# Performance work log

Measured on AMD Instinct MI355X. Metric: run time of the kernel, lower is better.

The kernel has to match this reference:

```python
import jax, jax.numpy as jnp
import numpy as np

N_NODES = 100000
N_EDGES = 800000
N_GRAPHS = 256
IN_C = 96
HID = 96
OUT_C = 16


def setup_inputs() -> dict:
    key = jax.random.key(0)
    ks = jax.random.split(key, 10)
    x = jax.random.normal(ks[0], (N_NODES, IN_C), dtype=jnp.float32)
    edge_index = jax.random.randint(ks[1], (2, N_EDGES), 0, N_NODES, dtype=jnp.int64)
    batch = jnp.sort(jax.random.randint(ks[2], (N_NODES,), 0, N_GRAPHS, dtype=jnp.int64))
    def glorot(k, fan_in, fan_out):
        s = np.sqrt(6.0 / (fan_in + fan_out)).astype(np.float32)
        return jax.random.uniform(k, (fan_in, fan_out), minval=-s, maxval=s, dtype=jnp.float32)
    W1 = glorot(ks[3], IN_C, HID)
    W2 = glorot(ks[4], HID, HID)
    W3 = glorot(ks[5], HID, HID)
    Wlin = glorot(ks[6], HID, OUT_C)
    b1 = jnp.zeros((HID,), dtype=jnp.float32)
    b2 = jnp.zeros((HID,), dtype=jnp.float32)
    b3 = jnp.zeros((HID,), dtype=jnp.float32)
    return {"x": x, "edge_index": edge_index, "batch": batch,
            "W1": W1, "b1": b1, "W2": W2, "b2": b2, "W3": W3, "b3": b3, "Wlin": Wlin}


def _gcn_conv(x, W, b, src, dst):
    # PyG GCNConv(normalize=True): add self-loops, deg includes self-loop,
    # norm_ij = deg_i^{-1/2} * deg_j^{-1/2}; linear (no bias) then scatter-add; bias after.
    n = x.shape[0]
    deg = jnp.zeros((n,), dtype=x.dtype).at[dst].add(1.0) + 1.0  # +1 self-loop
    dinv = jax.lax.rsqrt(deg)
    h = x @ W                                   # [N, H]
    coef = dinv[src] * dinv[dst]                # [E]
    msg = h[src] * coef[:, None]                # [E, H] gather
    agg = jax.ops.segment_sum(msg, dst, num_segments=n)  # scatter-add
    agg = agg + h * (dinv * dinv)[:, None]      # self-loop contribution
    return agg + b


def reference(x, edge_index, batch, W1, b1, W2, b2, W3, b3, Wlin):
    src, dst = edge_index[0], edge_index[1]
    h = jax.nn.relu(_gcn_conv(x, W1, b1, src, dst))
    h = jax.nn.relu(_gcn_conv(h, W2, b2, src, dst))
    h = _gcn_conv(h, W3, b3, src, dst)
    # global mean pool over graphs
    sums = jax.ops.segment_sum(h, batch, num_segments=N_GRAPHS)
    counts = jax.ops.segment_sum(jnp.ones((h.shape[0],), dtype=h.dtype), batch, num_segments=N_GRAPHS)
    pooled = sums / jnp.maximum(counts, 1.0)[:, None]
    return pooled @ Wlin
```

## Files before the change

kernel.cpp:

```cpp
#include <hip/hip_runtime.h>

#define NN 100000
#define NE 800000
#define NG 256
#define CH 96
#define OC 16
#define NBLK 391
#define TM 128
#define WPAD 104

typedef __attribute__((ext_vector_type(8))) short bf16x8;
typedef __attribute__((ext_vector_type(4))) float f32x4;

__global__ __launch_bounds__(256) void k_hist(const int* __restrict__ dst,
                                              int* __restrict__ cnt,
                                              int* __restrict__ slot) {
    int e = blockIdx.x * 256 + threadIdx.x;
    slot[e] = atomicAdd(&cnt[dst[e]], 1);
}

__global__ __launch_bounds__(256) void k_scan1(const int* __restrict__ cnt,
                                               int* __restrict__ off,
                                               int* __restrict__ bsum) {
    __shared__ int sh[256];
    int t = threadIdx.x;
    int i = blockIdx.x * 256 + t;
    int v = (i < NN) ? cnt[i] : 0;
    sh[t] = v;
    __syncthreads();
    for (int d = 1; d < 256; d <<= 1) {
        int x = (t >= d) ? sh[t - d] : 0;
        __syncthreads();
        sh[t] += x;
        __syncthreads();
    }
    if (i < NN) off[i] = sh[t] - v;
    if (t == 255) bsum[blockIdx.x] = sh[255];
}

__global__ __launch_bounds__(512) void k_scan2(int* __restrict__ bsum,
                                               int* __restrict__ boff) {
    __shared__ int sh[512];
    int t = threadIdx.x;
    int v = (t < NBLK) ? bsum[t] : 0;
    sh[t] = v;
    __syncthreads();
    for (int d = 1; d < 512; d <<= 1) {
        int x = (t >= d) ? sh[t - d] : 0;
        __syncthreads();
        sh[t] += x;
        __syncthreads();
    }
    if (t < NBLK) boff[t] = sh[t] - v;
}

__global__ __launch_bounds__(256) void k_scan3(const int* __restrict__ cnt,
                                               int* __restrict__ off,
                                               const int* __restrict__ boff,
                                               float* __restrict__ dinv,
                                               const int* __restrict__ batch,
                                               int* __restrict__ goff) {
    int i = blockIdx.x * 256 + threadIdx.x;
    if (i >= NN) return;
    off[i] += boff[i >> 8];
    dinv[i] = rsqrtf((float)cnt[i] + 1.0f);
    int b = batch[i];
    int bp = (i > 0) ? batch[i - 1] : -1;
    for (int g = bp + 1; g <= b; g++) goff[g] = i;
    if (i == NN - 1)
        for (int g = b + 1; g <= NG; g++) goff[g] = NN;
}

__global__ __launch_bounds__(256) void k_build(const int* __restrict__ src,
                                               const int* __restrict__ dst,
                                               const int* __restrict__ off,
                                               const int* __restrict__ slot,
                                               const float* __restrict__ dinv,
                                               float2* __restrict__ packed) {
    int e = blockIdx.x * 256 + threadIdx.x;
    int s = src[e];
    int d = dst[e];
    packed[off[d] + slot[e]] = make_float2(__int_as_float(s), dinv[s] * dinv[d]);
}

__device__ __forceinline__ unsigned short f2bf(float x) {
    unsigned u = __float_as_uint(x);
    return (unsigned short)((u + 0x7fffu + ((u >> 16) & 1u)) >> 16);
}
__device__ __forceinline__ float bf2f(unsigned short h) {
    return __uint_as_float(((unsigned)h) << 16);
}

__device__ __forceinline__ void split8(const float4 a, const float4 b,
                                       bf16x8& hi, bf16x8& lo) {
    float v[8] = {a.x, a.y, a.z, a.w, b.x, b.y, b.z, b.w};
#pragma unroll
    for (int j = 0; j < 8; j++) {
        unsigned short h = f2bf(v[j]);
        hi[j] = (short)h;
        lo[j] = (short)f2bf(v[j] - bf2f(h));
    }
}

__global__ __launch_bounds__(256) void k_gemm96(const float* __restrict__ X,
                                                const float* __restrict__ W,
                                                unsigned short* __restrict__ H) {
    __shared__ unsigned short WtHi[CH * WPAD];
    __shared__ unsigned short WtLo[CH * WPAD];

    const int tid = threadIdx.x;
    const int n0 = blockIdx.x * TM;

    {
        const float4* W4 = reinterpret_cast<const float4*>(W);
#pragma unroll
        for (int i = 0; i < 9; i++) {
            int f4 = tid * 9 + i;
            int k = f4 / 24;
            int nn = (f4 - k * 24) * 4;
            float4 v = W4[f4];
            float vv[4] = {v.x, v.y, v.z, v.w};
#pragma unroll
            for (int e = 0; e < 4; e++) {
                unsigned short h = f2bf(vv[e]);
                WtHi[(nn + e) * WPAD + k] = h;
                WtLo[(nn + e) * WPAD + k] = f2bf(vv[e] - bf2f(h));
            }
        }
    }
    __syncthreads();

    const int lane = tid & 63;
    const int wave = tid >> 6;
    const int lrow = lane & 15;
    const int quad = lane >> 4;

    const float4* X4 = reinterpret_cast<const float4*>(X);

    f32x4 acc[2][6];
#pragma unroll
    for (int rt = 0; rt < 2; rt++)
#pragma unroll
        for (int ct = 0; ct < 6; ct++) acc[rt][ct] = (f32x4){0.f, 0.f, 0.f, 0.f};

    int arow[2];
#pragma unroll
    for (int rt = 0; rt < 2; rt++)
        arow[rt] = min(n0 + (wave * 2 + rt) * 16 + lrow, NN - 1);

#pragma unroll
    for (int kc = 0; kc < 3; kc++) {
        bf16x8 ahi[2], alo[2];
#pragma unroll
        for (int rt = 0; rt < 2; rt++) {
            int fo = (arow[rt] * CH + kc * 32 + quad * 8) >> 2;
            split8(X4[fo], X4[fo + 1], ahi[rt], alo[rt]);
        }
#pragma unroll
        for (int ct = 0; ct < 6; ct++) {
            int bo = (ct * 16 + lrow) * WPAD + kc * 32 + quad * 8;
            bf16x8 bhi = *reinterpret_cast<const bf16x8*>(&WtHi[bo]);
            bf16x8 blo = *reinterpret_cast<const bf16x8*>(&WtLo[bo]);
#pragma unroll
            for (int rt = 0; rt < 2; rt++) {
                acc[rt][ct] = __builtin_amdgcn_mfma_f32_16x16x32_bf16(
                    alo[rt], bhi, acc[rt][ct], 0, 0, 0);
                acc[rt][ct] = __builtin_amdgcn_mfma_f32_16x16x32_bf16(
                    ahi[rt], blo, acc[rt][ct], 0, 0, 0);
                acc[rt][ct] = __builtin_amdgcn_mfma_f32_16x16x32_bf16(
                    ahi[rt], bhi, acc[rt][ct], 0, 0, 0);
            }
        }
    }

#pragma unroll
    for (int rt = 0; rt < 2; rt++) {
        int rbase = n0 + (wave * 2 + rt) * 16 + quad * 4;
#pragma unroll
        for (int ct = 0; ct < 6; ct++) {
            int col = ct * 16 + lrow;
#pragma unroll
            for (int r = 0; r < 4; r++) {
                int row = rbase + r;
                if (row < NN) H[(size_t)row * CH + col] = f2bf(acc[rt][ct][r]);
            }
        }
    }
}

__device__ __forceinline__ float4 us4_to_f4(ushort4 u) {
    return make_float4(bf2f(u.x), bf2f(u.y), bf2f(u.z), bf2f(u.w));
}

template <bool RELU>
__global__ __launch_bounds__(256) void k_aggregate(const int* __restrict__ off,
                                                   const float2* __restrict__ packed,
                                                   const float* __restrict__ dinv,
                                                   const float* __restrict__ bias,
                                                   const unsigned short* __restrict__ H,
                                                   float* __restrict__ B) {
    int idx = blockIdx.x * 256 + threadIdx.x;
    int n = idx / 24;
    int c4 = idx - n * 24;
    int e0 = off[n];
    int e1 = (n + 1 < NN) ? off[n + 1] : NE;

    const ushort4* H4 = reinterpret_cast<const ushort4*>(H);
    float di = dinv[n];
    float d2 = di * di;
    float4 h = us4_to_f4(H4[(size_t)n * 24 + c4]);
    float4 bb = reinterpret_cast<const float4*>(bias)[c4];
    float4 acc = make_float4(h.x * d2 + bb.x, h.y * d2 + bb.y,
                             h.z * d2 + bb.z, h.w * d2 + bb.w);

    int e = e0;
    for (; e + 4 <= e1; e += 4) {
        float2 p0 = packed[e + 0];
        float2 p1 = packed[e + 1];
        float2 p2 = packed[e + 2];
        float2 p3 = packed[e + 3];
        float4 v0 = us4_to_f4(H4[(size_t)__float_as_int(p0.x) * 24 + c4]);
        float4 v1 = us4_to_f4(H4[(size_t)__float_as_int(p1.x) * 24 + c4]);
        float4 v2 = us4_to_f4(H4[(size_t)__float_as_int(p2.x) * 24 + c4]);
        float4 v3 = us4_to_f4(H4[(size_t)__float_as_int(p3.x) * 24 + c4]);
        acc.x += v0.x * p0.y + v1.x * p1.y + v2.x * p2.y + v3.x * p3.y;
        acc.y += v0.y * p0.y + v1.y * p1.y + v2.y * p2.y + v3.y * p3.y;
        acc.z += v0.z * p0.y + v1.z * p1.y + v2.z * p2.y + v3.z * p3.y;
        acc.w += v0.w * p0.y + v1.w * p1.y + v2.w * p2.y + v3.w * p3.y;
    }
    for (; e < e1; e++) {
        float2 pc = packed[e];
        float4 v = us4_to_f4(H4[(size_t)__float_as_int(pc.x) * 24 + c4]);
        acc.x += v.x * pc.y; acc.y += v.y * pc.y;
        acc.z += v.z * pc.y; acc.w += v.w * pc.y;
    }
    if (RELU) {
        acc.x = fmaxf(acc.x, 0.0f); acc.y = fmaxf(acc.y, 0.0f);
        acc.z = fmaxf(acc.z, 0.0f); acc.w = fmaxf(acc.w, 0.0f);
    }
    reinterpret_cast<float4*>(B)[(size_t)n * 24 + c4] = acc;
}

__global__ __launch_bounds__(384) void k_pool_linear(const int* __restrict__ goff,
                                                     const float* __restrict__ B,
                                                     const float* __restrict__ Wlin,
                                                     float* __restrict__ out) {
    __shared__ float4 sh[16][24];
    __shared__ float pooled[CH];
    int g = blockIdx.x;
    int t = threadIdx.x;
    int nl = t / 24;
    int c4 = t - nl * 24;
    int s = goff[g];
    int e = goff[g + 1];

    float4 acc = make_float4(0.f, 0.f, 0.f, 0.f);
    const float4* B4 = reinterpret_cast<const float4*>(B);
    for (int n = s + nl; n < e; n += 16) {
        float4 v = B4[(size_t)n * 24 + c4];
        acc.x += v.x; acc.y += v.y; acc.z += v.z; acc.w += v.w;
    }
    sh[nl][c4] = acc;
    __syncthreads();

    if (t < 24) {
        float4 r = make_float4(0.f, 0.f, 0.f, 0.f);
#pragma unroll
        for (int j = 0; j < 16; j++) {
            float4 v = sh[j][t];
            r.x += v.x; r.y += v.y; r.z += v.z; r.w += v.w;
        }
        float inv = 1.0f / fmaxf((float)(e - s), 1.0f);
        pooled[t * 4 + 0] = r.x * inv;
        pooled[t * 4 + 1] = r.y * inv;
        pooled[t * 4 + 2] = r.z * inv;
        pooled[t * 4 + 3] = r.w * inv;
    }
    __syncthreads();

    if (t < OC) {
        float a = 0.0f;
#pragma unroll 8
        for (int k = 0; k < CH; k++) a += pooled[k] * Wlin[k * OC + t];
        out[g * OC + t] = a;
    }
}

extern "C" void kernel_launch(void* const* d_in, const int* in_sizes, int n_in,
                              void* d_out, int out_size, void* d_ws, size_t ws_size,
                              hipStream_t stream) {
    const float* x = (const float*)d_in[0];
    const int* ei = (const int*)d_in[1];
    const int* src = ei;
    const int* dst = ei + NE;
    const int* batch = (const int*)d_in[2];
    const float* W1 = (const float*)d_in[3];
    const float* b1 = (const float*)d_in[4];
    const float* W2 = (const float*)d_in[5];
    const float* b2 = (const float*)d_in[6];
    const float* W3 = (const float*)d_in[7];
    const float* b3 = (const float*)d_in[8];
    const float* Wlin = (const float*)d_in[9];
    float* out = (float*)d_out;

    char* ws = (char*)d_ws;
    unsigned short* H = (unsigned short*)ws;  ws += (size_t)NN * CH * 2;
    float* B = (float*)ws;         ws += (size_t)NN * CH * 4;
    float2* packed = (float2*)ws;  ws += (size_t)NE * 8;
    float* dinv = (float*)ws;      ws += NN * 4;
    int* cnt = (int*)ws;           ws += NN * 4;
    int* off = (int*)ws;           ws += NN * 4;
    int* bsum = (int*)ws;          ws += 512 * 4;
    int* boff = (int*)ws;          ws += 512 * 4;
    int* goff = (int*)ws;          ws += (NG + 1) * 4;
    int* slot = (int*)B;

    hipMemsetAsync(cnt, 0, NN * 4, stream);
    k_hist<<<NE / 256, 256, 0, stream>>>(dst, cnt, slot);
    k_scan1<<<NBLK, 256, 0, stream>>>(cnt, off, bsum);
    k_scan2<<<1, 512, 0, stream>>>(bsum, boff);
    k_scan3<<<NBLK, 256, 0, stream>>>(cnt, off, boff, dinv, batch, goff);
    k_build<<<NE / 256, 256, 0, stream>>>(src, dst, off, slot, dinv, packed);

    const int gblk = (NN + TM - 1) / TM;

    k_gemm96<<<gblk, 256, 0, stream>>>(x, W1, H);
    k_aggregate<true><<<NN * 24 / 256, 256, 0, stream>>>(off, packed, dinv, b1, H, B);

    k_gemm96<<<gblk, 256, 0, stream>>>(B, W2, H);
    k_aggregate<true><<<NN * 24 / 256, 256, 0, stream>>>(off, packed, dinv, b2, H, B);

    k_gemm96<<<gblk, 256, 0, stream>>>(B, W3, H);
    k_aggregate<false><<<NN * 24 / 256, 256, 0, stream>>>(off, packed, dinv, b3, H, B);

    k_pool_linear<<<NG, 384, 0, stream>>>(goff, B, Wlin, out);
}
```

Before: 321.6 us.

## Fuse aggregation with next layer GEMM and precompute split bf16 weights

Each hidden layer's scatter-aggregate plus ReLU now writes a 64-node tile into shared memory, and the same block immediately runs the next layer's MFMA GEMM on it. This removes the fp32 B round trip to global memory and two kernel launches. Weight hi/lo bf16 splitting and transposing is done once in a prep kernel, so per-block LDS staging of W is dropped and B fragments are read straight from global memory. The cost is global reads of the weights per block and fewer rows per block in the fused GEMM.

```diff
diff --git a/kernel.cpp b/kernel.cpp
--- a/kernel.cpp
+++ b/kernel.cpp
@@ -7,7 +7,8 @@
 #define OC 16
 #define NBLK 391
 #define TM 128
-#define WPAD 104
+#define FT 64
+#define RS 100
 
 typedef __attribute__((ext_vector_type(8))) short bf16x8;
 typedef __attribute__((ext_vector_type(4))) float f32x4;
@@ -90,7 +91,6 @@
 __device__ __forceinline__ float bf2f(unsigned short h) {
     return __uint_as_float(((unsigned)h) << 16);
 }
-
 __device__ __forceinline__ void split8(const float4 a, const float4 b,
                                        bf16x8& hi, bf16x8& lo) {
     float v[8] = {a.x, a.y, a.z, a.w, b.x, b.y, b.z, b.w};
@@ -101,35 +101,34 @@
         lo[j] = (short)f2bf(v[j] - bf2f(h));
     }
 }
+__device__ __forceinline__ float4 us4_to_f4(ushort4 u) {
+    return make_float4(bf2f(u.x), bf2f(u.y), bf2f(u.z), bf2f(u.w));
+}
+
+__global__ __launch_bounds__(256) void k_prep(const float* __restrict__ W1,
+                                              const float* __restrict__ W2,
+                                              const float* __restrict__ W3,
+                                              unsigned short* __restrict__ WH,
+                                              unsigned short* __restrict__ WL) {
+    int id = blockIdx.x * 256 + threadIdx.x;
+    if (id >= 3 * CH * CH) return;
+    int w = id / (CH * CH);
+    int r = id - w * CH * CH;
+    int k = r / CH;
+    int n = r - k * CH;
+    const float* Ws = (w == 0) ? W1 : (w == 1) ? W2 : W3;
+    float v = Ws[k * CH + n];
+    unsigned short h = f2bf(v);
+    WH[w * CH * CH + n * CH + k] = h;
+    WL[w * CH * CH + n * CH + k] = f2bf(v - bf2f(h));
+}
 
 __global__ __launch_bounds__(256) void k_gemm96(const float* __restrict__ X,
-                                                const float* __restrict__ W,
+                                                const unsigned short* __restrict__ WH,
+                                                const unsigned short* __restrict__ WL,
                                                 unsigned short* __restrict__ H) {
-    __shared__ unsigned short WtHi[CH * WPAD];
-    __shared__ unsigned short WtLo[CH * WPAD];
-
     const int tid = threadIdx.x;
     const int n0 = blockIdx.x * TM;
-
-    {
-        const float4* W4 = reinterpret_cast<const float4*>(W);
-#pragma unroll
-        for (int i = 0; i < 9; i++) {
-            int f4 = tid * 9 + i;
-            int k = f4 / 24;
-            int nn = (f4 - k * 24) * 4;
-            float4 v = W4[f4];
-            float vv[4] = {v.x, v.y, v.z, v.w};
-#pragma unroll
-            for (int e = 0; e < 4; e++) {
-                unsigned short h = f2bf(vv[e]);
-                WtHi[(nn + e) * WPAD + k] = h;
-                WtLo[(nn + e) * WPAD + k] = f2bf(vv[e] - bf2f(h));
-            }
-        }
-    }
-    __syncthreads();
-
     const int lane = tid & 63;
     const int wave = tid >> 6;
     const int lrow = lane & 15;
@@ -158,9 +157,9 @@
         }
 #pragma unroll
         for (int ct = 0; ct < 6; ct++) {
-            int bo = (ct * 16 + lrow) * WPAD + kc * 32 + quad * 8;
-            bf16x8 bhi = *reinterpret_cast<const bf16x8*>(&WtHi[bo]);
-            bf16x8 blo = *reinterpret_cast<const bf16x8*>(&WtLo[bo]);
+            int bo = (ct * 16 + lrow) * CH + kc * 32 + quad * 8;
+            bf16x8 bhi = *reinterpret_cast<const bf16x8*>(&WH[bo]);
+            bf16x8 blo = *reinterpret_cast<const bf16x8*>(&WL[bo]);
 #pragma unroll
             for (int rt = 0; rt < 2; rt++) {
                 acc[rt][ct] = __builtin_amdgcn_mfma_f32_16x16x32_bf16(
@@ -188,11 +187,102 @@
     }
 }
 
-__device__ __forceinline__ float4 us4_to_f4(ushort4 u) {
-    return make_float4(bf2f(u.x), bf2f(u.y), bf2f(u.z), bf2f(u.w));
-}
-
-template <bool RELU>
+__global__ __launch_bounds__(256) void k_fused(const int* __restrict__ off,
+                                               const float2* __restrict__ packed,
+                                               const float* __restrict__ dinv,
+                                               const float* __restrict__ bias,
+                                               const unsigned short* __restrict__ Hin,
+                                               const unsigned short* __restrict__ WH,
+                                               const unsigned short* __restrict__ WL,
+                                               unsigned short* __restrict__ Hout) {
+    __shared__ __align__(16) float Bs[FT * RS];
+
+    const int tid = threadIdx.x;
+    const int n0 = blockIdx.x * FT;
+    const ushort4* H4 = reinterpret_cast<const ushort4*>(Hin);
+
+    for (int it = tid; it < FT * 24; it += 256) {
+        int nl = it / 24;
+        int c4 = it - nl * 24;
+        int n = n0 + nl;
+        float4 acc = make_float4(0.f, 0.f, 0.f, 0.f);
+        if (n < NN) {
+            float di = dinv[n];
+            float d2 = di * di;
+            float4 h = us4_to_f4(H4[(size_t)n * 24 + c4]);
+            float4 bb = reinterpret_cast<const float4*>(bias)[c4];
+            acc = make_float4(h.x * d2 + bb.x, h.y * d2 + bb.y,
+                              h.z * d2 + bb.z, h.w * d2 + bb.w);
+            int e0 = off[n];
+            int e1 = (n + 1 < NN) ? off[n + 1] : NE;
+            int e = e0;
+            for (; e + 4 <= e1; e += 4) {
+                float2 p0 = packed[e + 0];
+                float2 p1 = packed[e + 1];
+                float2 p2 = packed[e + 2];
+                float2 p3 = packed[e + 3];
+                float4 v0 = us4_to_f4(H4[(size_t)__float_as_int(p0.x) * 24 + c4]);
+                float4 v1 = us4_to_f4(H4[(size_t)__float_as_int(p1.x) * 24 + c4]);
+                float4 v2 = us4_to_f4(H4[(size_t)__float_as_int(p2.x) * 24 + c4]);
+                float4 v3 = us4_to_f4(H4[(size_t)__float_as_int(p3.x) * 24 + c4]);
+                acc.x += v0.x * p0.y + v1.x * p1.y + v2.x * p2.y + v3.x * p3.y;
+                acc.y += v0.y * p0.y + v1.y * p1.y + v2.y * p2.y + v3.y * p3.y;
+                acc.z += v0.z * p0.y + v1.z * p1.y + v2.z * p2.y + v3.z * p3.y;
+                acc.w += v0.w * p0.y + v1.w * p1.y + v2.w * p2.y + v3.w * p3.y;
+            }
+            for (; e < e1; e++) {
+                float2 pc = packed[e];
+                float4 v = us4_to_f4(H4[(size_t)__float_as_int(pc.x) * 24 + c4]);
+                acc.x += v.x * pc.y; acc.y += v.y * pc.y;
+                acc.z += v.z * pc.y; acc.w += v.w * pc.y;
+            }
+            acc.x = fmaxf(acc.x, 0.0f); acc.y = fmaxf(acc.y, 0.0f);
+            acc.z = fmaxf(acc.z, 0.0f); acc.w = fmaxf(acc.w, 0.0f);
+        }
+        *reinterpret_cast<float4*>(&Bs[nl * RS + c4 * 4]) = acc;
+    }
+    __syncthreads();
+
+    const int lane = tid & 63;
+    const int wave = tid >> 6;
+    const int lrow = lane & 15;
+    const int quad = lane >> 4;
+
+    f32x4 acc[6];
+#pragma unroll
+    for (int ct = 0; ct < 6; ct++) acc[ct] = (f32x4){0.f, 0.f, 0.f, 0.f};
+
+    const int abase = (wave * 16 + lrow) * RS;
+#pragma unroll
+    for (int kc = 0; kc < 3; kc++) {
+        const float* ap = &Bs[abase + kc * 32 + quad * 8];
+        float4 a0 = *reinterpret_cast<const float4*>(ap);
+        float4 a1 = *reinterpret_cast<const float4*>(ap + 4);
+        bf16x8 ahi, alo;
+        split8(a0, a1, ahi, alo);
+#pragma unroll
+        for (int ct = 0; ct < 6; ct++) {
+            int bo = (ct * 16 + lrow) * CH + kc * 32 + quad * 8;
+            bf16x8 bhi = *reinterpret_cast<const bf16x8*>(&WH[bo]);
+            bf16x8 blo = *reinterpret_cast<const bf16x8*>(&WL[bo]);
+            acc[ct] = __builtin_amdgcn_mfma_f32_16x16x32_bf16(alo, bhi, acc[ct], 0, 0, 0);
+            acc[ct] = __builtin_amdgcn_mfma_f32_16x16x32_bf16(ahi, blo, acc[ct], 0, 0, 0);
+            acc[ct] = __builtin_amdgcn_mfma_f32_16x16x32_bf16(ahi, bhi, acc[ct], 0, 0, 0);
+        }
+    }
+
+    int rbase = n0 + wave * 16 + quad * 4;
+#pragma unroll
+    for (int ct = 0; ct < 6; ct++) {
+        int col = ct * 16 + lrow;
+#pragma unroll
+        for (int r = 0; r < 4; r++) {
+            int row = rbase + r;
+            if (row < NN) Hout[(size_t)row * CH + col] = f2bf(acc[ct][r]);
+        }
+    }
+}
+
 __global__ __launch_bounds__(256) void k_aggregate(const int* __restrict__ off,
                                                    const float2* __restrict__ packed,
                                                    const float* __restrict__ dinv,
@@ -233,10 +323,6 @@
         float4 v = us4_to_f4(H4[(size_t)__float_as_int(pc.x) * 24 + c4]);
         acc.x += v.x * pc.y; acc.y += v.y * pc.y;
         acc.z += v.z * pc.y; acc.w += v.w * pc.y;
-    }
-    if (RELU) {
-        acc.x = fmaxf(acc.x, 0.0f); acc.y = fmaxf(acc.y, 0.0f);
-        acc.z = fmaxf(acc.z, 0.0f); acc.w = fmaxf(acc.w, 0.0f);
     }
     reinterpret_cast<float4*>(B)[(size_t)n * 24 + c4] = acc;
 }
@@ -304,7 +390,8 @@
     float* out = (float*)d_out;
 
     char* ws = (char*)d_ws;
-    unsigned short* H = (unsigned short*)ws;  ws += (size_t)NN * CH * 2;
+    unsigned short* Ha = (unsigned short*)ws;  ws += (size_t)NN * CH * 2;
+    unsigned short* Hb = (unsigned short*)ws;  ws += (size_t)NN * CH * 2;
     float* B = (float*)ws;         ws += (size_t)NN * CH * 4;
     float2* packed = (float2*)ws;  ws += (size_t)NE * 8;
     float* dinv = (float*)ws;      ws += NN * 4;
@@ -312,6 +399,8 @@
     int* off = (int*)ws;           ws += NN * 4;
     int* bsum = (int*)ws;          ws += 512 * 4;
     int* boff = (int*)ws;          ws += 512 * 4;
+    unsigned short* WH = (unsigned short*)ws;  ws += 3 * CH * CH * 2;
+    unsigned short* WL = (unsigned short*)ws;  ws += 3 * CH * CH * 2;
     int* goff = (int*)ws;          ws += (NG + 1) * 4;
     int* slot = (int*)B;
 
@@ -321,17 +410,14 @@
     k_scan2<<<1, 512, 0, stream>>>(bsum, boff);
     k_scan3<<<NBLK, 256, 0, stream>>>(cnt, off, boff, dinv, batch, goff);
     k_build<<<NE / 256, 256, 0, stream>>>(src, dst, off, slot, dinv, packed);
-
-    const int gblk = (NN + TM - 1) / TM;
-
-    k_gemm96<<<gblk, 256, 0, stream>>>(x, W1, H);
-    k_aggregate<true><<<NN * 24 / 256, 256, 0, stream>>>(off, packed, dinv, b1, H, B);
-
-    k_gemm96<<<gblk, 256, 0, stream>>>(B, W2, H);
-    k_aggregate<true><<<NN * 24 / 256, 256, 0, stream>>>(off, packed, dinv, b2, H, B);
-
-    k_gemm96<<<gblk, 256, 0, stream>>>(B, W3, H);
-    k_aggregate<false><<<NN * 24 / 256, 256, 0, stream>>>(off, packed, dinv, b3, H, B);
+    k_prep<<<(3 * CH * CH + 255) / 256, 256, 0, stream>>>(W1, W2, W3, WH, WL);
+
+    k_gemm96<<<(NN + TM - 1) / TM, 256, 0, stream>>>(x, WH, WL, Ha);
+    k_fused<<<(NN + FT - 1) / FT, 256, 0, stream>>>(off, packed, dinv, b1, Ha,
+                                                    WH + CH * CH, WL + CH * CH, Hb);
+    k_fused<<<(NN + FT - 1) / FT, 256, 0, stream>>>(off, packed, dinv, b2, Hb,
+                                                    WH + 2 * CH * CH, WL + 2 * CH * CH, Ha);
+    k_aggregate<<<NN * 24 / 256, 256, 0, stream>>>(off, packed, dinv, b3, Ha, B);
 
     k_pool_linear<<<NG, 384, 0, stream>>>(goff, B, Wlin, out);
 }
```

Result: slower. 353.3 us (+9.9%).
